# Performance work log

Measured on AMD Instinct MI355X. Metric: run time of the kernel, lower is better.

Reference implementation:

```python
import jax, jax.numpy as jnp
import numpy as np

N, M, D = 16384, 16384, 16
MAX_NORM = 0.7  # keep points strictly inside Poincare ball

def _to_ball(v):
    # rescale so every point has norm < MAX_NORM
    n = jnp.linalg.norm(v, axis=1, keepdims=True)
    return MAX_NORM * v / (1.0 + n)

def setup_inputs() -> dict:
    key = jax.random.key(0)
    k1, k2 = jax.random.split(key)
    set1 = _to_ball(jax.random.normal(k1, (N, D), dtype=jnp.float32))
    set2 = _to_ball(jax.random.normal(k2, (M, D), dtype=jnp.float32))
    return {"set1": set1, "set2": set2}

def hypcdist(x, y, epsilon=0.0):
    # ||x_i - y_j||^2 for all pairs: [N, M]
    diff = x[:, None, :] - y[None, :, :]
    sqdist = jnp.sum(diff * diff, axis=-1)
    x_norm = jnp.sum(x * x, axis=1)[:, None]   # [N,1]
    y_norm = jnp.sum(y * y, axis=1)[None, :]   # [1,M]
    u = 1.0 + 2.0 * sqdist / ((1.0 - x_norm) * (1.0 - y_norm)) + epsilon
    v = jnp.sqrt(u * u - 1.0)
    return jnp.log(u + v)  # arcosh(u)

def reference(set1, set2):
    d2 = hypcdist(set1, set2)                 # [N, M]
    term_1 = jnp.mean(jnp.min(d2, axis=1))    # for each point in set1, nearest in set2
    term_2 = jnp.mean(jnp.min(d2, axis=0))    # for each point in set2, nearest in set1
    return term_1 + term_2                    # directed=False
```

## Files before the change

kernel.cpp:

```cpp
#include <hip/hip_runtime.h>
#include <math.h>

#define NPTS 16384
#define DIM  16
#define KH   32
#define CSPLIT 16
#define COLS_PER_BLOCK (NPTS / CSPLIT)
#define JT_TOTAL (COLS_PER_BLOCK / 16)
#define ROWS_PER_BLOCK 512
#define RBLK (NPTS / ROWS_PER_BLOCK)
#define MT 8
#define NBLOCKS (2 * RBLK * CSPLIT)

typedef _Float16 f16x8 __attribute__((ext_vector_type(8)));
typedef float    f32x4 __attribute__((ext_vector_type(4)));

__global__ __launch_bounds__(256) void prep_kernel(const float* __restrict__ s1,
                                                   const float* __restrict__ s2,
                                                   _Float16* __restrict__ Xp,
                                                   _Float16* __restrict__ Yp,
                                                   unsigned int* __restrict__ rowfinal,
                                                   float* __restrict__ out) {
    int b = blockIdx.x, tid = threadIdx.x;
    int idx = b * 256 + tid;
    rowfinal[idx] = 0xFFFFFFFFu;
    if (idx == 0) out[0] = 0.f;

    int isX = (b < 64);
    const float* src = isX ? s1 : s2;
    _Float16* dst = isX ? Xp : Yp;
    int p = (isX ? b : b - 64) * 256 + tid;

    const float4* s4 = (const float4*)(src + (size_t)p * DIM);
    float4 A = s4[0], B = s4[1], C = s4[2], D = s4[3];
    float v[DIM] = {A.x,A.y,A.z,A.w, B.x,B.y,B.z,B.w,
                    C.x,C.y,C.z,C.w, D.x,D.y,D.z,D.w};
    float n2 = 0.f;
#pragma unroll
    for (int k = 0; k < DIM; ++k) n2 = fmaf(v[k], v[k], n2);
    float r = 1.0f / (1.0f - n2);
    float a[18];
#pragma unroll
    for (int k = 0; k < DIM; ++k) a[k] = r * v[k];
    if (isX) { a[16] = -0.5f * r * n2; a[17] = r; }
    else     { a[16] = r;              a[17] = -0.5f * r * n2; }

    __attribute__((aligned(16))) _Float16 buf[KH];
#pragma unroll
    for (int k = 0; k < 18; ++k) buf[k] = (_Float16)a[k];
#pragma unroll
    for (int k = 18; k < KH; ++k) buf[k] = (_Float16)0.f;

    int g = p >> 4, c = p & 15;
    const uint4* b4 = (const uint4*)buf;
#pragma unroll
    for (int q = 0; q < 4; ++q) {
        size_t off = (size_t)g * 512 + (size_t)q * 128 + (size_t)c * 8;
        *(uint4*)(dst + off) = b4[q];
    }
}

__global__ __launch_bounds__(256, 2) void pairs_kernel(const _Float16* __restrict__ Xp,
                                                       const _Float16* __restrict__ Yp,
                                                       unsigned int* __restrict__ rowfinal) {
    __shared__ __align__(16) _Float16 Bs[COLS_PER_BLOCK * KH];

    const int b = blockIdx.x;
    const int pass = b >> 9;
    const int within = b & 511;
    const int r  = within >> 4;
    const int cs = within & 15;

    const _Float16* Aset = pass ? Yp : Xp;
    const _Float16* Bset = pass ? Xp : Yp;
    unsigned int* outMin = rowfinal + pass * NPTS;

    const int tid = threadIdx.x;
    const int lane = tid & 63, w = tid >> 6;
    const int c = lane & 15, quad = lane >> 4;

    {
        const char* gsrc = (const char*)Bset + (size_t)cs * (COLS_PER_BLOCK * KH * 2)
                         + (size_t)tid * 16;
        char* lb = (char*)Bs + (size_t)tid * 16;
#pragma unroll
        for (int e = 0; e < 16; ++e) {
            __builtin_amdgcn_global_load_lds(
                (const __attribute__((address_space(1))) unsigned int*)(gsrc + e * 4096),
                (__attribute__((address_space(3))) unsigned int*)(lb + e * 4096),
                16, 0, 0);
        }
    }

    f16x8 af[MT];
#pragma unroll
    for (int t = 0; t < MT; ++t) {
        int g = r * 32 + w * 8 + t;
        af[t] = *(const f16x8*)&Aset[(size_t)g * 512 + (size_t)lane * 8];
    }

    f32x4 rowmax[MT];
#pragma unroll
    for (int t = 0; t < MT; ++t)
        rowmax[t] = (f32x4){-INFINITY, -INFINITY, -INFINITY, -INFINITY};

    const f32x4 zero = (f32x4){0.f, 0.f, 0.f, 0.f};

    __syncthreads();

#pragma unroll 4
    for (int jt = 0; jt < JT_TOTAL; ++jt) {
        f16x8 bf = *(const f16x8*)&Bs[jt * 512 + lane * 8];
#pragma unroll
        for (int t = 0; t < MT; ++t) {
            f32x4 acc = __builtin_amdgcn_mfma_f32_16x16x32_f16(af[t], bf, zero, 0, 0, 0);
            rowmax[t][0] = fmaxf(rowmax[t][0], acc[0]);
            rowmax[t][1] = fmaxf(rowmax[t][1], acc[1]);
            rowmax[t][2] = fmaxf(rowmax[t][2], acc[2]);
            rowmax[t][3] = fmaxf(rowmax[t][3], acc[3]);
        }
    }

#pragma unroll
    for (int t = 0; t < MT; ++t) {
#pragma unroll
        for (int e = 0; e < 4; ++e) {
            float m = rowmax[t][e];
            m = fmaxf(m, __shfl_xor(m, 1, 64));
            m = fmaxf(m, __shfl_xor(m, 2, 64));
            m = fmaxf(m, __shfl_xor(m, 4, 64));
            m = fmaxf(m, __shfl_xor(m, 8, 64));
            if (c == 0) {
                int row = ((r * 32 + w * 8 + t) << 4) + quad * 4 + e;
                atomicMin(&outMin[row], __float_as_uint(m));
            }
        }
    }
}

__global__ __launch_bounds__(256) void finalize_kernel(const unsigned int* __restrict__ rowfinal,
                                                       float* __restrict__ out) {
    int idx = blockIdx.x * 256 + threadIdx.x;
    float f = __uint_as_float(rowfinal[idx]);
    float t = fmaxf(-4.0f * f, 0.0f);
    float d = log1pf(t + sqrtf(t * (t + 2.0f)));
    float val = d * (1.0f / NPTS);

    __shared__ float sred[256];
    sred[threadIdx.x] = val;
    __syncthreads();
    for (int s = 128; s > 0; s >>= 1) {
        if (threadIdx.x < s) sred[threadIdx.x] += sred[threadIdx.x + s];
        __syncthreads();
    }
    if (threadIdx.x == 0) atomicAdd(out, sred[0]);
}

extern "C" void kernel_launch(void* const* d_in, const int* in_sizes, int n_in,
                              void* d_out, int out_size, void* d_ws, size_t ws_size,
                              hipStream_t stream) {
    const float* set1 = (const float*)d_in[0];
    const float* set2 = (const float*)d_in[1];
    float* out = (float*)d_out;

    _Float16* Xp = (_Float16*)d_ws;
    _Float16* Yp = Xp + (size_t)NPTS * KH;
    unsigned int* rowfinal = (unsigned int*)(Yp + (size_t)NPTS * KH);

    prep_kernel<<<128, 256, 0, stream>>>(set1, set2, Xp, Yp, rowfinal, out);
    pairs_kernel<<<NBLOCKS, 256, 0, stream>>>(Xp, Yp, rowfinal);
    finalize_kernel<<<2 * NPTS / 256, 256, 0, stream>>>(rowfinal, out);
}
```

Measured before the change: 92.56 us.

## Compute row and column minima in one pass over the pair matrix

Replaces the two passes over the pair matrix (X×Y for row minima and Y×X for column minima) with a single pass. Each MFMA tile now feeds both the per-row max registers and a per-column max, which is reduced across quads with shuffles. The column value is then merged into a block-local LDS array with atomicMin and flushed to global memory at the end. This halves the MFMA work and the block count, at the cost of extra VALU max operations, shuffles and one LDS atomic per column tile in the inner loop. The loop unroll factor also drops from 4 to 2.

Result: no change. 93.92 us (+1.5%).

```diff
diff --git a/kernel.cpp b/kernel.cpp
--- a/kernel.cpp
+++ b/kernel.cpp
@@ -10,15 +10,15 @@
 #define ROWS_PER_BLOCK 512
 #define RBLK (NPTS / ROWS_PER_BLOCK)
 #define MT 8
-#define NBLOCKS (2 * RBLK * CSPLIT)
+#define NBLOCKS (RBLK * CSPLIT)
 
 typedef _Float16 f16x8 __attribute__((ext_vector_type(8)));
 typedef float    f32x4 __attribute__((ext_vector_type(4)));
 
 __global__ __launch_bounds__(256) void prep_kernel(const float* __restrict__ s1,
                                                    const float* __restrict__ s2,
-                                                   _Float16* __restrict__ Xp,
-                                                   _Float16* __restrict__ Yp,
+                                                   _Float16* __restrict__ Xa,
+                                                   _Float16* __restrict__ Yb,
                                                    unsigned int* __restrict__ rowfinal,
                                                    float* __restrict__ out) {
     int b = blockIdx.x, tid = threadIdx.x;
@@ -28,7 +28,7 @@
 
     int isX = (b < 64);
     const float* src = isX ? s1 : s2;
-    _Float16* dst = isX ? Xp : Yp;
+    _Float16* dst = isX ? Xa : Yb;
     int p = (isX ? b : b - 64) * 256 + tid;
 
     const float4* s4 = (const float4*)(src + (size_t)p * DIM);
@@ -39,15 +39,12 @@
 #pragma unroll
     for (int k = 0; k < DIM; ++k) n2 = fmaf(v[k], v[k], n2);
     float r = 1.0f / (1.0f - n2);
-    float a[18];
-#pragma unroll
-    for (int k = 0; k < DIM; ++k) a[k] = r * v[k];
-    if (isX) { a[16] = -0.5f * r * n2; a[17] = r; }
-    else     { a[16] = r;              a[17] = -0.5f * r * n2; }
 
     __attribute__((aligned(16))) _Float16 buf[KH];
 #pragma unroll
-    for (int k = 0; k < 18; ++k) buf[k] = (_Float16)a[k];
+    for (int k = 0; k < DIM; ++k) buf[k] = (_Float16)(r * v[k]);
+    if (isX) { buf[16] = (_Float16)(0.5f * r * n2);  buf[17] = (_Float16)r; }
+    else     { buf[16] = (_Float16)(-r);             buf[17] = (_Float16)(-0.5f * r * n2); }
 #pragma unroll
     for (int k = 18; k < KH; ++k) buf[k] = (_Float16)0.f;
 
@@ -60,27 +57,24 @@
     }
 }
 
-__global__ __launch_bounds__(256, 2) void pairs_kernel(const _Float16* __restrict__ Xp,
-                                                       const _Float16* __restrict__ Yp,
+__global__ __launch_bounds__(256, 2) void pairs_kernel(const _Float16* __restrict__ Xa,
+                                                       const _Float16* __restrict__ Yb,
                                                        unsigned int* __restrict__ rowfinal) {
     __shared__ __align__(16) _Float16 Bs[COLS_PER_BLOCK * KH];
+    __shared__ unsigned int colLDS[COLS_PER_BLOCK];
 
     const int b = blockIdx.x;
-    const int pass = b >> 9;
-    const int within = b & 511;
-    const int r  = within >> 4;
-    const int cs = within & 15;
+    const int r  = b >> 4;
+    const int cs = b & 15;
 
-    const _Float16* Aset = pass ? Yp : Xp;
-    const _Float16* Bset = pass ? Xp : Yp;
-    unsigned int* outMin = rowfinal + pass * NPTS;
+    unsigned int* colfinal = rowfinal + NPTS;
 
     const int tid = threadIdx.x;
     const int lane = tid & 63, w = tid >> 6;
     const int c = lane & 15, quad = lane >> 4;
 
     {
-        const char* gsrc = (const char*)Bset + (size_t)cs * (COLS_PER_BLOCK * KH * 2)
+        const char* gsrc = (const char*)Yb + (size_t)cs * (COLS_PER_BLOCK * KH * 2)
                          + (size_t)tid * 16;
         char* lb = (char*)Bs + (size_t)tid * 16;
 #pragma unroll
@@ -91,12 +85,14 @@
                 16, 0, 0);
         }
     }
+#pragma unroll
+    for (int e = 0; e < 4; ++e) colLDS[tid + e * 256] = 0xFFFFFFFFu;
 
     f16x8 af[MT];
 #pragma unroll
     for (int t = 0; t < MT; ++t) {
         int g = r * 32 + w * 8 + t;
-        af[t] = *(const f16x8*)&Aset[(size_t)g * 512 + (size_t)lane * 8];
+        af[t] = *(const f16x8*)&Xa[(size_t)g * 512 + (size_t)lane * 8];
     }
 
     f32x4 rowmax[MT];
@@ -108,9 +104,10 @@
 
     __syncthreads();
 
-#pragma unroll 4
+#pragma unroll 2
     for (int jt = 0; jt < JT_TOTAL; ++jt) {
         f16x8 bf = *(const f16x8*)&Bs[jt * 512 + lane * 8];
+        float cm = -INFINITY;
 #pragma unroll
         for (int t = 0; t < MT; ++t) {
             f32x4 acc = __builtin_amdgcn_mfma_f32_16x16x32_f16(af[t], bf, zero, 0, 0, 0);
@@ -118,7 +115,13 @@
             rowmax[t][1] = fmaxf(rowmax[t][1], acc[1]);
             rowmax[t][2] = fmaxf(rowmax[t][2], acc[2]);
             rowmax[t][3] = fmaxf(rowmax[t][3], acc[3]);
+            float cv = fmaxf(fmaxf(acc[0], acc[1]), fmaxf(acc[2], acc[3]));
+            cm = fmaxf(cm, cv);
         }
+        cm = fmaxf(cm, __shfl_xor(cm, 16, 64));
+        cm = fmaxf(cm, __shfl_xor(cm, 32, 64));
+        if (quad == 0)
+            atomicMin(&colLDS[jt * 16 + c], __float_as_uint(cm));
     }
 
 #pragma unroll
@@ -132,9 +135,16 @@
             m = fmaxf(m, __shfl_xor(m, 8, 64));
             if (c == 0) {
                 int row = ((r * 32 + w * 8 + t) << 4) + quad * 4 + e;
-                atomicMin(&outMin[row], __float_as_uint(m));
+                atomicMin(&rowfinal[row], __float_as_uint(m));
             }
         }
+    }
+
+    __syncthreads();
+#pragma unroll
+    for (int e = 0; e < 4; ++e) {
+        int i = tid + e * 256;
+        atomicMin(&colfinal[cs * COLS_PER_BLOCK + i], colLDS[i]);
     }
 }
 
@@ -163,11 +173,11 @@
     const float* set2 = (const float*)d_in[1];
     float* out = (float*)d_out;
 
-    _Float16* Xp = (_Float16*)d_ws;
-    _Float16* Yp = Xp + (size_t)NPTS * KH;
-    unsigned int* rowfinal = (unsigned int*)(Yp + (size_t)NPTS * KH);
+    _Float16* Xa = (_Float16*)d_ws;
+    _Float16* Yb = Xa + (size_t)NPTS * KH;
+    unsigned int* rowfinal = (unsigned int*)(Yb + (size_t)NPTS * KH);
 
-    prep_kernel<<<128, 256, 0, stream>>>(set1, set2, Xp, Yp, rowfinal, out);
-    pairs_kernel<<<NBLOCKS, 256, 0, stream>>>(Xp, Yp, rowfinal);
+    prep_kernel<<<128, 256, 0, stream>>>(set1, set2, Xa, Yb, rowfinal, out);
+    pairs_kernel<<<NBLOCKS, 256, 0, stream>>>(Xa, Yb, rowfinal);
     finalize_kernel<<<2 * NPTS / 256, 256, 0, stream>>>(rowfinal, out);
 }
```
